# Kernel tuning notes

Hardware: AMD Instinct MI355X
Metric: run time of the kernel (lower is better)

The kernel has to match this reference:

```python
import jax, jax.numpy as jnp
import numpy as np

B, N, C, H = 2, 2048, 768, 12
DH = C // H
SCALE = DH ** (-0.5)


def setup_inputs() -> dict:
    key = jax.random.key(0)
    k1, k2, k3, k4 = jax.random.split(key, 4)
    x = jax.random.normal(k1, (B, N, 1, C), dtype=jnp.float32)
    mask = jax.random.randint(k2, (B, N), 0, 2) > 0  # bool keep-mask
    w_qkv = jax.random.normal(k3, (3 * C, C), dtype=jnp.float32) * (C ** -0.5)
    w_proj = jax.random.normal(k4, (C, C), dtype=jnp.float32) * (C ** -0.5)
    b_proj = jnp.zeros((C,), dtype=jnp.float32)
    return {"x": x, "mask": mask, "w_qkv": w_qkv, "w_proj": w_proj, "b_proj": b_proj}


def reference(x, mask, w_qkv, w_proj, b_proj):
    Bs, N1, N2, Cs = x.shape  # N2 == 1 required by the original reshape
    # qkv: Linear(dim, 3*dim, bias=False) -> reshape (B,N1,3,H,Dh) -> (3,B,H,N1,Dh)
    qkv = jnp.einsum('bnoc,dc->bnod', x, w_qkv)  # (B,N1,1,3C)
    qkv = qkv.reshape(Bs, N1, 3, H, Cs // H).transpose(2, 0, 3, 1, 4)
    q, k, v = qkv[0], qkv[1], qkv[2]  # each (B,H,N,Dh)
    attn = jnp.einsum('bhid,bhjd->bhij', q, k) * SCALE  # (B,H,N,N)
    mask_value = -jnp.finfo(attn.dtype).max
    pair = mask[:, None, :] & mask[:, :, None]  # (B,N,N), broadcast over heads
    attn = jnp.where(pair[:, None, :, :], attn, mask_value)
    attn = jax.nn.softmax(attn, axis=-1)
    # dropout in eval mode -> identity
    out = jnp.einsum('bhij,bhjd->bhid', attn, v)  # (B,H,N,Dh)
    out = out.transpose(0, 2, 1, 3).reshape(Bs, N1, Cs)  # (B,N,C)
    out = out @ w_proj.T + b_proj
    return out
```

## Files before the change

### kernel.cpp

```cpp
#include <hip/hip_runtime.h>

#define BB 2
#define NN 2048
#define CC 768
#define HH 12
#define DHH 64
#define SCALE 0.125f

typedef __attribute__((ext_vector_type(4))) float f32x4;
typedef __attribute__((ext_vector_type(8))) short short8;
typedef __attribute__((ext_vector_type(4))) unsigned short u16x4;
typedef __attribute__((ext_vector_type(8))) unsigned short u16x8;

static __device__ __forceinline__ unsigned short f2bf(float f) {
    unsigned int u = __float_as_uint(f);
    u += 0x7FFFu + ((u >> 16) & 1u);
    return (unsigned short)(u >> 16);
}

union FragU {
    u16x4 u4[2];
    u16x8 u8;
    unsigned short us[8];
    short8 s8;
};

__global__ void cvt_f32_bf16(const float* __restrict__ in,
                             unsigned short* __restrict__ out, int n8) {
    int i = blockIdx.x * blockDim.x + threadIdx.x;
    if (i >= n8) return;
    const f32x4* p = (const f32x4*)(in + (size_t)i * 8);
    f32x4 a = p[0], b = p[1];
    u16x8 o;
    o[0] = f2bf(a[0]); o[1] = f2bf(a[1]); o[2] = f2bf(a[2]); o[3] = f2bf(a[3]);
    o[4] = f2bf(b[0]); o[5] = f2bf(b[1]); o[6] = f2bf(b[2]); o[7] = f2bf(b[3]);
    *(u16x8*)(out + (size_t)i * 8) = o;
}

__launch_bounds__(256)
__global__ void gemm_bt(const unsigned short* __restrict__ A,
                        const unsigned short* __restrict__ Bt,
                        unsigned short* __restrict__ outB,
                        float* __restrict__ outF,
                        const float* __restrict__ bias,
                        int M, int N, int K) {
    __shared__ __align__(16) unsigned short As[128][40];
    __shared__ __align__(16) unsigned short Bs[128][40];
    int tid = threadIdx.x;
    int lane = tid & 63;
    int w = tid >> 6;
    int wm = w >> 1, wn = w & 1;
    int bn = blockIdx.x, bm = blockIdx.y;
    int li = lane & 15, g = lane >> 4;

    f32x4 acc[4][4] = {};
    const unsigned short* Abase = A + (size_t)(bm * 128) * K;
    const unsigned short* Bbase = Bt + (size_t)(bn * 128) * K;

    for (int k0 = 0; k0 < K; k0 += 32) {
#pragma unroll
        for (int s = 0; s < 2; ++s) {
            int q = tid + s * 256;
            int row = q >> 2, c0 = (q & 3) * 8;
            *(u16x8*)&As[row][c0] = *(const u16x8*)&Abase[(size_t)row * K + k0 + c0];
            *(u16x8*)&Bs[row][c0] = *(const u16x8*)&Bbase[(size_t)row * K + k0 + c0];
        }
        __syncthreads();
        FragU a[4], b[4];
#pragma unroll
        for (int mi = 0; mi < 4; ++mi) {
            int r = wm * 64 + mi * 16 + li;
            a[mi].u4[0] = *(const u16x4*)&As[r][g * 4];
            a[mi].u4[1] = *(const u16x4*)&As[r][g * 4 + 16];
        }
#pragma unroll
        for (int ni = 0; ni < 4; ++ni) {
            int r = wn * 64 + ni * 16 + li;
            b[ni].u4[0] = *(const u16x4*)&Bs[r][g * 4];
            b[ni].u4[1] = *(const u16x4*)&Bs[r][g * 4 + 16];
        }
#pragma unroll
        for (int mi = 0; mi < 4; ++mi)
#pragma unroll
            for (int ni = 0; ni < 4; ++ni)
                acc[mi][ni] = __builtin_amdgcn_mfma_f32_16x16x32_bf16(
                    a[mi].s8, b[ni].s8, acc[mi][ni], 0, 0, 0);
        __syncthreads();
    }

#pragma unroll
    for (int mi = 0; mi < 4; ++mi) {
#pragma unroll
        for (int ni = 0; ni < 4; ++ni) {
#pragma unroll
            for (int r = 0; r < 4; ++r) {
                int row = bm * 128 + wm * 64 + mi * 16 + g * 4 + r;
                int col = bn * 128 + wn * 64 + ni * 16 + li;
                float v = acc[mi][ni][r];
                if (outB) outB[(size_t)row * N + col] = f2bf(v);
                else      outF[(size_t)row * N + col] = v + bias[col];
            }
        }
    }
}

__launch_bounds__(256)
__global__ void attn_kernel(const unsigned short* __restrict__ qkv,
                            const int* __restrict__ mask,
                            unsigned short* __restrict__ hout) {
    __shared__ __align__(16) unsigned short Ks[32][72];
    __shared__ __align__(16) unsigned short Vt[64][36];
    __shared__ unsigned long long mbits[32];

    int tid = threadIdx.x;
    int lane = tid & 63;
    int w = tid >> 6;
    int li = lane & 15, g = lane >> 4;

    int qb = blockIdx.x & 31;
    int bh = blockIdx.x >> 5;
    int b = bh / HH, head = bh % HH;

#pragma unroll
    for (int r = 0; r < 8; ++r) {
        int j = r * 256 + w * 64 + lane;
        unsigned long long bal = __ballot(mask[b * NN + j] != 0);
        if (lane == 0) mbits[r * 4 + w] = bal;
    }

    int qrow = qb * 64 + w * 16 + li;
    size_t qoff = ((size_t)(b * NN + qrow)) * 2304 + head * DHH;
    FragU qf[2];
#pragma unroll
    for (int d0 = 0; d0 < 2; ++d0) {
        qf[d0].u4[0] = *(const u16x4*)&qkv[qoff + d0 * 32 + g * 4];
        qf[d0].u4[1] = *(const u16x4*)&qkv[qoff + d0 * 32 + g * 4 + 16];
    }
    bool rk = mask[b * NN + qrow] != 0;
    float m_st = rk ? -1e30f : 0.0f;
    float l_st = 0.0f;
    f32x4 acc[4] = {};

    int krow = tid >> 3, kc0 = (tid & 7) * 8;
    size_t kbase = ((size_t)(b * NN)) * 2304 + CC + head * DHH;
    size_t vbase = ((size_t)(b * NN)) * 2304 + 2 * CC + head * DHH;

    for (int kb = 0; kb < NN; kb += 32) {
        __syncthreads();
        *(u16x8*)&Ks[krow][kc0] =
            *(const u16x8*)&qkv[kbase + (size_t)(kb + krow) * 2304 + kc0];
        u16x8 vv = *(const u16x8*)&qkv[vbase + (size_t)(kb + krow) * 2304 + kc0];
#pragma unroll
        for (int e = 0; e < 8; ++e) Vt[kc0 + e][krow] = vv[e];
        __syncthreads();

        f32x4 st[2];
#pragma unroll
        for (int t = 0; t < 2; ++t) {
            FragU kf0, kf1;
            kf0.u4[0] = *(const u16x4*)&Ks[t * 16 + li][g * 4];
            kf0.u4[1] = *(const u16x4*)&Ks[t * 16 + li][g * 4 + 16];
            kf1.u4[0] = *(const u16x4*)&Ks[t * 16 + li][32 + g * 4];
            kf1.u4[1] = *(const u16x4*)&Ks[t * 16 + li][32 + g * 4 + 16];
            f32x4 z = {};
            z = __builtin_amdgcn_mfma_f32_16x16x32_bf16(kf0.s8, qf[0].s8, z, 0, 0, 0);
            z = __builtin_amdgcn_mfma_f32_16x16x32_bf16(kf1.s8, qf[1].s8, z, 0, 0, 0);
            st[t] = z;
        }

        unsigned kbits[2];
#pragma unroll
        for (int t = 0; t < 2; ++t) {
            int j0 = kb + t * 16 + g * 4;
            kbits[t] = (unsigned)((mbits[j0 >> 6] >> (j0 & 63)) & 15ull);
        }
        float sv[2][4];
        bool pz[2][4];
        float tmax = -1e38f;
#pragma unroll
        for (int t = 0; t < 2; ++t)
#pragma unroll
            for (int r = 0; r < 4; ++r) {
                float s = st[t][r] * SCALE;
                bool ck = (kbits[t] >> r) & 1u;
                sv[t][r] = rk ? s : 0.0f;
                pz[t][r] = rk && !ck;
                float cand = rk ? (ck ? s : -1e30f) : 0.0f;
                tmax = fmaxf(tmax, cand);
            }
        tmax = fmaxf(tmax, __shfl_xor(tmax, 16));
        tmax = fmaxf(tmax, __shfl_xor(tmax, 32));
        float mnew = fmaxf(m_st, tmax);
        float alpha = __expf(m_st - mnew);
        float lsum = 0.0f;
        FragU pf;
#pragma unroll
        for (int t = 0; t < 2; ++t)
#pragma unroll
            for (int r = 0; r < 4; ++r) {
                float pv = pz[t][r] ? 0.0f : __expf(sv[t][r] - mnew);
                lsum += pv;
                pf.us[t * 4 + r] = f2bf(pv);
            }
        lsum += __shfl_xor(lsum, 16);
        lsum += __shfl_xor(lsum, 32);
        l_st = l_st * alpha + lsum;
        m_st = mnew;

        float ar[4];
#pragma unroll
        for (int r = 0; r < 4; ++r) ar[r] = __shfl(alpha, g * 4 + r);
#pragma unroll
        for (int dt = 0; dt < 4; ++dt)
#pragma unroll
            for (int r = 0; r < 4; ++r) acc[dt][r] *= ar[r];

#pragma unroll
        for (int dt = 0; dt < 4; ++dt) {
            FragU vf;
            vf.u4[0] = *(const u16x4*)&Vt[dt * 16 + li][g * 4];
            vf.u4[1] = *(const u16x4*)&Vt[dt * 16 + li][g * 4 + 16];
            acc[dt] = __builtin_amdgcn_mfma_f32_16x16x32_bf16(pf.s8, vf.s8, acc[dt], 0, 0, 0);
        }
    }

    float linv = 1.0f / l_st;
    float lr[4];
#pragma unroll
    for (int r = 0; r < 4; ++r) lr[r] = __shfl(linv, g * 4 + r);
#pragma unroll
    for (int dt = 0; dt < 4; ++dt)
#pragma unroll
        for (int r = 0; r < 4; ++r) {
            int orow = qb * 64 + w * 16 + g * 4 + r;
            hout[((size_t)(b * NN + orow)) * CC + head * DHH + dt * 16 + li] =
                f2bf(acc[dt][r] * lr[r]);
        }
}

extern "C" void kernel_launch(void* const* d_in, const int* in_sizes, int n_in,
                              void* d_out, int out_size, void* d_ws, size_t ws_size,
                              hipStream_t stream) {
    const float* x     = (const float*)d_in[0];
    const int*   mask  = (const int*)d_in[1];
    const float* wqkv  = (const float*)d_in[2];
    const float* wproj = (const float*)d_in[3];
    const float* bproj = (const float*)d_in[4];
    float* out = (float*)d_out;

    unsigned short* x_bf     = (unsigned short*)d_ws;
    unsigned short* wqkv_bf  = x_bf + 3145728;
    unsigned short* wproj_bf = wqkv_bf + 1769472;
    unsigned short* qkv_bf   = wproj_bf + 589824;
    unsigned short* h_bf     = qkv_bf + 9437184;

    cvt_f32_bf16<<<1536, 256, 0, stream>>>(x, x_bf, 393216);
    cvt_f32_bf16<<<864, 256, 0, stream>>>(wqkv, wqkv_bf, 221184);
    cvt_f32_bf16<<<288, 256, 0, stream>>>(wproj, wproj_bf, 73728);

    gemm_bt<<<dim3(18, 32), 256, 0, stream>>>(x_bf, wqkv_bf, qkv_bf, nullptr,
                                              nullptr, 4096, 2304, 768);
    attn_kernel<<<768, 256, 0, stream>>>(qkv_bf, mask, h_bf);
    gemm_bt<<<dim3(6, 32), 256, 0, stream>>>(h_bf, wproj_bf, nullptr, out,
                                             bproj, 4096, 768, 768);
}
```

Measured before the change: 267.3 us.

## Rework GEMM and attention with async LDS loads, swizzling, double buffering and exp2

The GEMM now uses global_load_lds with XOR-swizzled 64-wide K tiles and setprio around the MFMAs. The QKV GEMM folds the softmax scale times log2(e) into Q so attention can use exp2. Attention processes 64-key tiles with double-buffered K/V, an additive mask penalty held in LDS, and a lazy rescale that runs only when the row max grows. Masked query rows are filled from a precomputed mean of V instead of running the uniform softmax. It also remaps blocks across XCDs and sets launch bounds to 3 blocks per CU. These changes target load latency, LDS bank conflicts and per-tile softmax overhead, but add an extra vmean kernel and more code complexity.

```diff
diff --git a/kernel.cpp b/kernel.cpp
--- a/kernel.cpp
+++ b/kernel.cpp
@@ -1,29 +1,38 @@
 #include <hip/hip_runtime.h>
 
-#define BB 2
 #define NN 2048
 #define CC 768
 #define HH 12
-#define DHH 64
-#define SCALE 0.125f
+#define SCALE2 0.18033688011112042f
+#define NEGB  -3.0e35f
 
 typedef __attribute__((ext_vector_type(4))) float f32x4;
 typedef __attribute__((ext_vector_type(8))) short short8;
-typedef __attribute__((ext_vector_type(4))) unsigned short u16x4;
 typedef __attribute__((ext_vector_type(8))) unsigned short u16x8;
 
+#if __has_builtin(__builtin_amdgcn_exp2f)
+#define EXP2(x) __builtin_amdgcn_exp2f(x)
+#else
+#define EXP2(x) exp2f(x)
+#endif
+
 static __device__ __forceinline__ unsigned short f2bf(float f) {
-    unsigned int u = __float_as_uint(f);
+    unsigned u = __float_as_uint(f);
     u += 0x7FFFu + ((u >> 16) & 1u);
     return (unsigned short)(u >> 16);
 }
 
-union FragU {
-    u16x4 u4[2];
-    u16x8 u8;
-    unsigned short us[8];
-    short8 s8;
-};
+static __device__ __forceinline__ f32x4 MFMA(u16x8 a, u16x8 b, f32x4 c) {
+    union { u16x8 u; short8 s; } ua, ub;
+    ua.u = a; ub.u = b;
+    return __builtin_amdgcn_mfma_f32_16x16x32_bf16(ua.s, ub.s, c, 0, 0, 0);
+}
+
+static __device__ __forceinline__ void glds16(const void* g, void* l) {
+    __builtin_amdgcn_global_load_lds(
+        (const __attribute__((address_space(1))) unsigned int*)g,
+        (__attribute__((address_space(3))) unsigned int*)l, 16, 0, 0);
+}
 
 __global__ void cvt_f32_bf16(const float* __restrict__ in,
                              unsigned short* __restrict__ out, int n8) {
@@ -43,49 +52,46 @@
                         unsigned short* __restrict__ outB,
                         float* __restrict__ outF,
                         const float* __restrict__ bias,
-                        int M, int N, int K) {
-    __shared__ __align__(16) unsigned short As[128][40];
-    __shared__ __align__(16) unsigned short Bs[128][40];
-    int tid = threadIdx.x;
-    int lane = tid & 63;
-    int w = tid >> 6;
+                        int M, int N, int K, int qcols) {
+    __shared__ __align__(16) unsigned short As[128][64];
+    __shared__ __align__(16) unsigned short Bs[128][64];
+    int tid = threadIdx.x, lane = tid & 63, w = tid >> 6;
     int wm = w >> 1, wn = w & 1;
+    int li = lane & 15, g = lane >> 4;
     int bn = blockIdx.x, bm = blockIdx.y;
-    int li = lane & 15, g = lane >> 4;
 
     f32x4 acc[4][4] = {};
-    const unsigned short* Abase = A + (size_t)(bm * 128) * K;
-    const unsigned short* Bbase = Bt + (size_t)(bn * 128) * K;
-
-    for (int k0 = 0; k0 < K; k0 += 32) {
-#pragma unroll
-        for (int s = 0; s < 2; ++s) {
-            int q = tid + s * 256;
-            int row = q >> 2, c0 = (q & 3) * 8;
-            *(u16x8*)&As[row][c0] = *(const u16x8*)&Abase[(size_t)row * K + k0 + c0];
-            *(u16x8*)&Bs[row][c0] = *(const u16x8*)&Bbase[(size_t)row * K + k0 + c0];
-        }
+
+    int lrow = lane >> 3, lsl = lane & 7;
+    int xcol = (lsl ^ (lrow & 7)) * 8;
+    const unsigned short* Ag = A  + (size_t)(bm * 128 + w * 32 + lrow) * K + xcol;
+    const unsigned short* Bg = Bt + (size_t)(bn * 128 + w * 32 + lrow) * K + xcol;
+
+    for (int k0 = 0; k0 < K; k0 += 64) {
         __syncthreads();
-        FragU a[4], b[4];
-#pragma unroll
-        for (int mi = 0; mi < 4; ++mi) {
-            int r = wm * 64 + mi * 16 + li;
-            a[mi].u4[0] = *(const u16x4*)&As[r][g * 4];
-            a[mi].u4[1] = *(const u16x4*)&As[r][g * 4 + 16];
-        }
-#pragma unroll
-        for (int ni = 0; ni < 4; ++ni) {
-            int r = wn * 64 + ni * 16 + li;
-            b[ni].u4[0] = *(const u16x4*)&Bs[r][g * 4];
-            b[ni].u4[1] = *(const u16x4*)&Bs[r][g * 4 + 16];
-        }
-#pragma unroll
-        for (int mi = 0; mi < 4; ++mi)
+#pragma unroll
+        for (int i = 0; i < 4; ++i) {
+            glds16(Ag + (size_t)(i * 8) * K + k0, &As[w * 32 + i * 8][0]);
+            glds16(Bg + (size_t)(i * 8) * K + k0, &Bs[w * 32 + i * 8][0]);
+        }
+        __syncthreads();
+#pragma unroll
+        for (int kk = 0; kk < 2; ++kk) {
+            u16x8 af[4], bf[4];
+#pragma unroll
+            for (int mi = 0; mi < 4; ++mi)
+                af[mi] = *(const u16x8*)&As[wm * 64 + mi * 16 + li][((4 * kk + g) ^ (li & 7)) * 8];
 #pragma unroll
             for (int ni = 0; ni < 4; ++ni)
-                acc[mi][ni] = __builtin_amdgcn_mfma_f32_16x16x32_bf16(
-                    a[mi].s8, b[ni].s8, acc[mi][ni], 0, 0, 0);
-        __syncthreads();
+                bf[ni] = *(const u16x8*)&Bs[wn * 64 + ni * 16 + li][((4 * kk + g) ^ (li & 7)) * 8];
+            __builtin_amdgcn_s_setprio(1);
+#pragma unroll
+            for (int mi = 0; mi < 4; ++mi)
+#pragma unroll
+                for (int ni = 0; ni < 4; ++ni)
+                    acc[mi][ni] = MFMA(af[mi], bf[ni], acc[mi][ni]);
+            __builtin_amdgcn_s_setprio(0);
+        }
     }
 
 #pragma unroll
@@ -97,145 +103,209 @@
                 int row = bm * 128 + wm * 64 + mi * 16 + g * 4 + r;
                 int col = bn * 128 + wn * 64 + ni * 16 + li;
                 float v = acc[mi][ni][r];
-                if (outB) outB[(size_t)row * N + col] = f2bf(v);
-                else      outF[(size_t)row * N + col] = v + bias[col];
+                if (outB) {
+                    if (col < qcols) v *= SCALE2;
+                    outB[(size_t)row * N + col] = f2bf(v);
+                } else {
+                    outF[(size_t)row * N + col] = v + bias[col];
+                }
             }
         }
     }
 }
 
 __launch_bounds__(256)
+__global__ void vmean_kernel(const unsigned short* __restrict__ qkv,
+                             float* __restrict__ vmean) {
+    __shared__ float red[4][64];
+    int bh = blockIdx.x;
+    int b = bh / HH, h = bh % HH;
+    int d = threadIdx.x & 63, c = threadIdx.x >> 6;
+    const unsigned short* base = qkv + (size_t)(b * NN) * 2304 + 2 * CC + h * 64 + d;
+    float s = 0.f;
+    for (int j = c; j < NN; j += 4)
+        s += __uint_as_float((unsigned)base[(size_t)j * 2304] << 16);
+    red[c][d] = s;
+    __syncthreads();
+    if (c == 0)
+        vmean[bh * 64 + d] = (red[0][d] + red[1][d] + red[2][d] + red[3][d]) * (1.0f / NN);
+}
+
+__launch_bounds__(256, 3)
 __global__ void attn_kernel(const unsigned short* __restrict__ qkv,
                             const int* __restrict__ mask,
+                            const float* __restrict__ vmean,
                             unsigned short* __restrict__ hout) {
-    __shared__ __align__(16) unsigned short Ks[32][72];
-    __shared__ __align__(16) unsigned short Vt[64][36];
-    __shared__ unsigned long long mbits[32];
+    __shared__ __align__(16) unsigned short Ks[2][64][64];
+    __shared__ __align__(16) unsigned int   Vp[2][64][32];
+    __shared__ __align__(16) float pen[NN];
 
     int tid = threadIdx.x;
     int lane = tid & 63;
     int w = tid >> 6;
     int li = lane & 15, g = lane >> 4;
 
-    int qb = blockIdx.x & 31;
-    int bh = blockIdx.x >> 5;
+    int lb = (blockIdx.x & 7) * 96 + (blockIdx.x >> 3);
+    int qb = lb & 31;
+    int bh = lb >> 5;
     int b = bh / HH, head = bh % HH;
-
-#pragma unroll
-    for (int r = 0; r < 8; ++r) {
-        int j = r * 256 + w * 64 + lane;
-        unsigned long long bal = __ballot(mask[b * NN + j] != 0);
-        if (lane == 0) mbits[r * 4 + w] = bal;
-    }
+    const int* mb = mask + b * NN;
+
+    {
+        int i = tid * 8;
+        union { int4 v; int a[4]; } m0, m1;
+        m0.v = *(const int4*)&mb[i];
+        m1.v = *(const int4*)&mb[i + 4];
+        f32x4 p0, p1;
+#pragma unroll
+        for (int r = 0; r < 4; ++r) {
+            p0[r] = m0.a[r] ? 0.f : NEGB;
+            p1[r] = m1.a[r] ? 0.f : NEGB;
+        }
+        *(f32x4*)&pen[i] = p0;
+        *(f32x4*)&pen[i + 4] = p1;
+    }
+
+    const unsigned short* qbase = qkv + (size_t)(b * NN) * 2304;
 
     int qrow = qb * 64 + w * 16 + li;
-    size_t qoff = ((size_t)(b * NN + qrow)) * 2304 + head * DHH;
-    FragU qf[2];
-#pragma unroll
-    for (int d0 = 0; d0 < 2; ++d0) {
-        qf[d0].u4[0] = *(const u16x4*)&qkv[qoff + d0 * 32 + g * 4];
-        qf[d0].u4[1] = *(const u16x4*)&qkv[qoff + d0 * 32 + g * 4 + 16];
-    }
-    bool rk = mask[b * NN + qrow] != 0;
-    float m_st = rk ? -1e30f : 0.0f;
-    float l_st = 0.0f;
+    const unsigned short* qp = qbase + (size_t)qrow * 2304 + head * 64;
+    u16x8 qf0 = *(const u16x8*)(qp + g * 8);
+    u16x8 qf1 = *(const u16x8*)(qp + 32 + g * 8);
+
+    int xslot = ((lane & 7) ^ ((lane >> 3) & 7)) * 8;
+    const unsigned short* kg = qbase + CC + head * 64 + xslot
+                               + (size_t)(w * 16 + (lane >> 3)) * 2304;
+
+    int vm = tid >> 3;
+    int vkc = (tid & 7) * 8;
+    int vcol = (vm & 16) | ((vm & 6) << 1) | ((vm & 8) >> 2) | (vm & 1);
+    int vslot = vcol >> 2, vsub = vcol & 3;
+    const unsigned short* vg = qbase + 2 * CC + head * 64 + vkc;
+
+    u16x8 va, vb;
+    auto stageK = [&](int buf, int kb) {
+        glds16(kg + (size_t)kb * 2304,       &Ks[buf][w * 16][0]);
+        glds16(kg + (size_t)(kb + 8) * 2304, &Ks[buf][w * 16 + 8][0]);
+    };
+    auto loadV = [&](int kb) {
+        va = *(const u16x8*)(vg + (size_t)(kb + 2 * vm) * 2304);
+        vb = *(const u16x8*)(vg + (size_t)(kb + 2 * vm + 1) * 2304);
+    };
+    auto writeV = [&](int buf) {
+        union { u16x8 v; unsigned u[4]; } ua, ub;
+        ua.v = va; ub.v = vb;
+        unsigned* vp = &Vp[buf][0][0];
+#pragma unroll
+        for (int e = 0; e < 8; ++e) {
+            int dd = (e + (tid & 7)) & 7;
+            unsigned dw = __builtin_amdgcn_perm(ub.u[dd >> 1], ua.u[dd >> 1],
+                                                (dd & 1) ? 0x07060302u : 0x05040100u);
+            int d0 = vkc + dd;
+            vp[d0 * 32 + ((vslot ^ (d0 & 7)) << 2) + vsub] = dw;
+        }
+    };
+
+    stageK(0, 0);
+    loadV(0);
+    writeV(0);
+
+    float m_st = -1e30f, l_st = 0.f;
     f32x4 acc[4] = {};
-
-    int krow = tid >> 3, kc0 = (tid & 7) * 8;
-    size_t kbase = ((size_t)(b * NN)) * 2304 + CC + head * DHH;
-    size_t vbase = ((size_t)(b * NN)) * 2304 + 2 * CC + head * DHH;
-
-    for (int kb = 0; kb < NN; kb += 32) {
+    int cur = 0;
+
+    for (int kb = 0; kb < NN; kb += 64) {
         __syncthreads();
-        *(u16x8*)&Ks[krow][kc0] =
-            *(const u16x8*)&qkv[kbase + (size_t)(kb + krow) * 2304 + kc0];
-        u16x8 vv = *(const u16x8*)&qkv[vbase + (size_t)(kb + krow) * 2304 + kc0];
-#pragma unroll
-        for (int e = 0; e < 8; ++e) Vt[kc0 + e][krow] = vv[e];
-        __syncthreads();
-
-        f32x4 st[2];
-#pragma unroll
-        for (int t = 0; t < 2; ++t) {
-            FragU kf0, kf1;
-            kf0.u4[0] = *(const u16x4*)&Ks[t * 16 + li][g * 4];
-            kf0.u4[1] = *(const u16x4*)&Ks[t * 16 + li][g * 4 + 16];
-            kf1.u4[0] = *(const u16x4*)&Ks[t * 16 + li][32 + g * 4];
-            kf1.u4[1] = *(const u16x4*)&Ks[t * 16 + li][32 + g * 4 + 16];
+        int nx = cur ^ 1;
+        bool more = (kb + 64 < NN);
+        if (more) { stageK(nx, kb + 64); loadV(kb + 64); }
+
+        f32x4 st[4];
+        __builtin_amdgcn_s_setprio(1);
+#pragma unroll
+        for (int t = 0; t < 4; ++t) {
+            const unsigned short* kr = &Ks[cur][t * 16 + li][0];
+            u16x8 k0 = *(const u16x8*)(kr + ((g ^ (li & 7)) * 8));
+            u16x8 k1 = *(const u16x8*)(kr + (((4 + g) ^ (li & 7)) * 8));
             f32x4 z = {};
-            z = __builtin_amdgcn_mfma_f32_16x16x32_bf16(kf0.s8, qf[0].s8, z, 0, 0, 0);
-            z = __builtin_amdgcn_mfma_f32_16x16x32_bf16(kf1.s8, qf[1].s8, z, 0, 0, 0);
+            z = MFMA(k0, qf0, z);
+            z = MFMA(k1, qf1, z);
             st[t] = z;
         }
-
-        unsigned kbits[2];
-#pragma unroll
-        for (int t = 0; t < 2; ++t) {
-            int j0 = kb + t * 16 + g * 4;
-            kbits[t] = (unsigned)((mbits[j0 >> 6] >> (j0 & 63)) & 15ull);
-        }
-        float sv[2][4];
-        bool pz[2][4];
-        float tmax = -1e38f;
-#pragma unroll
-        for (int t = 0; t < 2; ++t)
-#pragma unroll
-            for (int r = 0; r < 4; ++r) {
-                float s = st[t][r] * SCALE;
-                bool ck = (kbits[t] >> r) & 1u;
-                sv[t][r] = rk ? s : 0.0f;
-                pz[t][r] = rk && !ck;
-                float cand = rk ? (ck ? s : -1e30f) : 0.0f;
-                tmax = fmaxf(tmax, cand);
-            }
+        __builtin_amdgcn_s_setprio(0);
+
+        const float* pp = &pen[kb];
+        float tmax = -3.0e38f;
+#pragma unroll
+        for (int t = 0; t < 4; ++t) {
+            f32x4 p4 = *(const f32x4*)&pp[t * 16 + g * 4];
+            st[t] += p4;
+            tmax = fmaxf(tmax, fmaxf(fmaxf(st[t][0], st[t][1]),
+                                     fmaxf(st[t][2], st[t][3])));
+        }
         tmax = fmaxf(tmax, __shfl_xor(tmax, 16));
         tmax = fmaxf(tmax, __shfl_xor(tmax, 32));
-        float mnew = fmaxf(m_st, tmax);
-        float alpha = __expf(m_st - mnew);
-        float lsum = 0.0f;
-        FragU pf;
-#pragma unroll
-        for (int t = 0; t < 2; ++t)
-#pragma unroll
-            for (int r = 0; r < 4; ++r) {
-                float pv = pz[t][r] ? 0.0f : __expf(sv[t][r] - mnew);
-                lsum += pv;
-                pf.us[t * 4 + r] = f2bf(pv);
-            }
+        if (__any(tmax > m_st)) {
+            float mnew = fmaxf(m_st, tmax);
+            float alpha = EXP2(m_st - mnew);
+            float ar[4];
+#pragma unroll
+            for (int r = 0; r < 4; ++r) ar[r] = __shfl(alpha, g * 4 + r);
+#pragma unroll
+            for (int dt = 0; dt < 4; ++dt)
+#pragma unroll
+                for (int r = 0; r < 4; ++r) acc[dt][r] *= ar[r];
+            l_st *= alpha;
+            m_st = mnew;
+        }
+        float lsum = 0.f;
+        union { unsigned u[8]; u16x8 v[2]; } pu;
+#pragma unroll
+        for (int t = 0; t < 4; ++t) {
+            f32x4 e4;
+#pragma unroll
+            for (int r = 0; r < 4; ++r) { e4[r] = EXP2(st[t][r] - m_st); lsum += e4[r]; }
+            pu.u[t * 2]     = __builtin_amdgcn_perm(__float_as_uint(e4[1]),
+                                                    __float_as_uint(e4[0]), 0x07060302u);
+            pu.u[t * 2 + 1] = __builtin_amdgcn_perm(__float_as_uint(e4[3]),
+                                                    __float_as_uint(e4[2]), 0x07060302u);
+        }
         lsum += __shfl_xor(lsum, 16);
         lsum += __shfl_xor(lsum, 32);
-        l_st = l_st * alpha + lsum;
-        m_st = mnew;
-
-        float ar[4];
-#pragma unroll
-        for (int r = 0; r < 4; ++r) ar[r] = __shfl(alpha, g * 4 + r);
-#pragma unroll
-        for (int dt = 0; dt < 4; ++dt)
-#pragma unroll
-            for (int r = 0; r < 4; ++r) acc[dt][r] *= ar[r];
-
-#pragma unroll
-        for (int dt = 0; dt < 4; ++dt) {
-            FragU vf;
-            vf.u4[0] = *(const u16x4*)&Vt[dt * 16 + li][g * 4];
-            vf.u4[1] = *(const u16x4*)&Vt[dt * 16 + li][g * 4 + 16];
-            acc[dt] = __builtin_amdgcn_mfma_f32_16x16x32_bf16(pf.s8, vf.s8, acc[dt], 0, 0, 0);
-        }
+        l_st += lsum;
+
+        __builtin_amdgcn_s_setprio(1);
+#pragma unroll
+        for (int h = 0; h < 2; ++h) {
+#pragma unroll
+            for (int dt = 0; dt < 4; ++dt) {
+                const unsigned* vr = &Vp[cur][dt * 16 + li][0];
+                u16x8 vf = *(const u16x8*)(vr + (((4 * h + g) ^ (li & 7)) << 2));
+                acc[dt] = MFMA(pu.v[h], vf, acc[dt]);
+            }
+        }
+        __builtin_amdgcn_s_setprio(0);
+
+        if (more) writeV(nx);
+        cur = nx;
     }
 
     float linv = 1.0f / l_st;
     float lr[4];
 #pragma unroll
     for (int r = 0; r < 4; ++r) lr[r] = __shfl(linv, g * 4 + r);
-#pragma unroll
-    for (int dt = 0; dt < 4; ++dt)
+    union { int4 v; int a[4]; } mk;
+    mk.v = *(const int4*)&mb[qb * 64 + w * 16 + g * 4];
+    size_t obase = ((size_t)(b * NN + qb * 64 + w * 16)) * CC + head * 64;
+#pragma unroll
+    for (int dt = 0; dt < 4; ++dt) {
+        float vmv = vmean[bh * 64 + dt * 16 + li];
 #pragma unroll
         for (int r = 0; r < 4; ++r) {
-            int orow = qb * 64 + w * 16 + g * 4 + r;
-            hout[((size_t)(b * NN + orow)) * CC + head * DHH + dt * 16 + li] =
-                f2bf(acc[dt][r] * lr[r]);
-        }
+            float v = mk.a[r] ? acc[dt][r] * lr[r] : vmv;
+            hout[obase + (size_t)(g * 4 + r) * CC + dt * 16 + li] = f2bf(v);
+        }
+    }
 }
 
 extern "C" void kernel_launch(void* const* d_in, const int* in_sizes, int n_in,
@@ -253,14 +323,16 @@
     unsigned short* wproj_bf = wqkv_bf + 1769472;
     unsigned short* qkv_bf   = wproj_bf + 589824;
     unsigned short* h_bf     = qkv_bf + 9437184;
+    float*          vmean    = (float*)(h_bf + 3145728);
 
     cvt_f32_bf16<<<1536, 256, 0, stream>>>(x, x_bf, 393216);
     cvt_f32_bf16<<<864, 256, 0, stream>>>(wqkv, wqkv_bf, 221184);
     cvt_f32_bf16<<<288, 256, 0, stream>>>(wproj, wproj_bf, 73728);
 
     gemm_bt<<<dim3(18, 32), 256, 0, stream>>>(x_bf, wqkv_bf, qkv_bf, nullptr,
-                                              nullptr, 4096, 2304, 768);
-    attn_kernel<<<768, 256, 0, stream>>>(qkv_bf, mask, h_bf);
+                                              nullptr, 4096, 2304, 768, 768);
+    vmean_kernel<<<24, 256, 0, stream>>>(qkv_bf, vmean);
+    attn_kernel<<<768, 256, 0, stream>>>(qkv_bf, mask, vmean, h_bf);
     gemm_bt<<<dim3(6, 32), 256, 0, stream>>>(h_bf, wproj_bf, nullptr, out,
-                                             bproj, 4096, 768, 768);
-}
+                                             bproj, 4096, 768, 768, 0);
+}
```

After: 365.8 us. +36.9%, slower.
